# Optimization experiments

Hardware: AMD Instinct MI355X
Metric: run time of the kernel (lower is better)

The kernel has to match this reference:

```python
import jax, jax.numpy as jnp
import numpy as np

B, T, E, G, A, D, H1, H2 = 64, 500, 256, 256, 128, 400, 256, 128
MAX_STEPS, R = 500, 5


def setup_inputs() -> dict:
    key = jax.random.key(0)
    ks = jax.random.split(key, 12)
    s = lambda k, shape: jax.random.normal(k, shape, jnp.float32) * 0.05
    return dict(
        enc_feat=jax.random.normal(ks[0], (B, T, E), jnp.float32),
        W_p1=s(ks[1], (D, H1)), b_p1=jnp.zeros((H1,), jnp.float32),
        W_p2=s(ks[2], (H1, H2)), b_p2=jnp.zeros((H2,), jnp.float32),
        # GRU cell (input = prenet_out + context = H2+E)
        W_ix=s(ks[3], (H2 + E, 3 * G)), W_ih=s(ks[4], (G, 3 * G)),
        b_ix=jnp.zeros((3 * G,), jnp.float32), b_ih=jnp.zeros((3 * G,), jnp.float32),
        # Bahdanau MLP attention: v^T tanh(W_dec h + W_enc e + b)
        W_dec=s(ks[5], (G, A)), W_enc=s(ks[6], (E, A)),
        b_attn=jnp.zeros((A,), jnp.float32), v_attn=s(ks[7], (A,)),
        # output projection [G+E] -> D, softmaxed per R chunks
        W_out=s(ks[8], (G + E, D)), b_out=jnp.zeros((D,), jnp.float32),
    )


def reference(enc_feat, W_p1, b_p1, W_p2, b_p2, W_ix, W_ih, b_ix, b_ih,
              W_dec, W_enc, b_attn, v_attn, W_out, b_out):
    # precompute encoder-side attention projection once [B,T,A]
    enc_proj = enc_feat @ W_enc

    def gru_cell(x, h):
        gi = x @ W_ix + b_ix  # [B,3G]
        gh = h @ W_ih + b_ih
        i_r, i_z, i_n = jnp.split(gi, 3, axis=-1)
        h_r, h_z, h_n = jnp.split(gh, 3, axis=-1)
        r = jax.nn.sigmoid(i_r + h_r)
        z = jax.nn.sigmoid(i_z + h_z)
        n = jnp.tanh(i_n + r * h_n)
        return (1.0 - z) * n + z * h

    def step(carry, _):
        pred, h, context = carry
        # prenet (eval: no dropout)
        x = jax.nn.relu(jax.nn.relu(pred @ W_p1 + b_p1) @ W_p2 + b_p2)  # [B,H2]
        h = gru_cell(jnp.concatenate([x, context], axis=-1), h)  # [B,G]
        score = jnp.einsum('bta,a->bt',
                           jnp.tanh(enc_proj + (h @ W_dec + b_attn)[:, None, :]),
                           v_attn)  # [B,T]
        attn = jax.nn.softmax(score, axis=-1)
        context = jnp.einsum('bt,bte->be', attn, enc_feat)  # [B,E]
        raw = jnp.concatenate([h, context], axis=-1) @ W_out + b_out  # [B,D]
        pred = jax.nn.softmax(raw.reshape(B, R, D // R), axis=-1).reshape(B, D)
        return (pred, h, context), (pred, attn)

    init = (jnp.zeros((B, D), enc_feat.dtype),
            jnp.zeros((B, G), enc_feat.dtype),
            jnp.zeros((B, E), enc_feat.dtype))
    _, (pred_seq, attn_record) = jax.lax.scan(step, init, None, length=MAX_STEPS)
    # scan stacks on leading axis: [S,B,.] -> [B,S,.]
    return jnp.transpose(pred_seq, (1, 0, 2)), jnp.transpose(attn_record, (1, 0, 2))
```

## Files before the change

### kernel.cpp

```cpp
#include <hip/hip_runtime.h>
#include <math.h>

constexpr int Bb = 64, Tt = 500, Ee = 256, Gg = 256, Aa = 128, Dd = 400;
constexpr int H1 = 256, H2 = 128, STEPS = 500, Rr = 5;

__global__ __launch_bounds__(512)
void k_encproj(const float* __restrict__ enc_feat,
               const float* __restrict__ W_enc,
               float* __restrict__ enc_proj) {
  __shared__ float sFeat[16][256];
  const int b = blockIdx.x, tg = blockIdx.y;
  const int t0 = tg * 16;
  const int tid = threadIdx.x;

  #pragma unroll
  for (int i = 0; i < 8; ++i) {
    int idx = tid + i * 512;
    int r = idx >> 8, c = idx & 255;
    int t = t0 + r;
    sFeat[r][c] = (t < Tt) ? enc_feat[((size_t)b * Tt + t) * Ee + c] : 0.0f;
  }
  __syncthreads();

  const int a = tid & 127, tl = tid >> 7;
  float acc0 = 0.f, acc1 = 0.f, acc2 = 0.f, acc3 = 0.f;
  #pragma unroll 4
  for (int k = 0; k < Ee; ++k) {
    float w = W_enc[k * Aa + a];
    acc0 = fmaf(sFeat[tl][k],      w, acc0);
    acc1 = fmaf(sFeat[tl + 4][k],  w, acc1);
    acc2 = fmaf(sFeat[tl + 8][k],  w, acc2);
    acc3 = fmaf(sFeat[tl + 12][k], w, acc3);
  }
  float accs[4] = {acc0, acc1, acc2, acc3};
  #pragma unroll
  for (int i = 0; i < 4; ++i) {
    int t = t0 + tl + 4 * i;
    if (t < Tt) enc_proj[((size_t)b * Tt + t) * Aa + a] = accs[i];
  }
}


template<int QUADS, int KS>
__device__ __forceinline__ void gemv_partial(const float* __restrict__ W, const int ldW,
                                             const float* __restrict__ xl,
                                             float* __restrict__ sTmp, int tid) {
  const int q = tid & (QUADS - 1);
  const int s = tid / QUADS;
  const float* Wp = W + 4 * q + (size_t)(s * KS) * ldW;
  const float* xp = xl + s * KS;
  float4 acc = {0.f, 0.f, 0.f, 0.f};
  #pragma unroll 4
  for (int k = 0; k < KS; ++k) {
    float xv = xp[k];
    float4 w = *(const float4*)(Wp + (size_t)k * ldW);
    acc.x = fmaf(xv, w.x, acc.x);
    acc.y = fmaf(xv, w.y, acc.y);
    acc.z = fmaf(xv, w.z, acc.z);
    acc.w = fmaf(xv, w.w, acc.w);
  }
  *(float4*)&sTmp[tid * 4] = acc;
}

template<int QUADS, int NSL>
__device__ __forceinline__ float combine(const float* __restrict__ sTmp, int j) {
  float v = 0.f;
  #pragma unroll
  for (int s = 0; s < NSL; ++s)
    v += sTmp[(s * QUADS + (j >> 2)) * 4 + (j & 3)];
  return v;
}

__device__ __forceinline__ float sigmoid_acc(float x) {
  float e = __expf(-x);
  return 1.0f / (1.0f + e);
}

__device__ __forceinline__ float tanh_acc(float x) {
  float cx = fminf(9.5f, fmaxf(-9.5f, x));
  float e = __expf(2.0f * cx);
  return (e - 1.0f) / (e + 1.0f);
}

__device__ __forceinline__ float tanh_fast(float x) {
  float cx = fminf(9.5f, fmaxf(-9.5f, x));
  float e = __expf(2.0f * cx);
  return (e - 1.0f) * __builtin_amdgcn_rcpf(e + 1.0f);
}

__global__ __launch_bounds__(512, 1)
void k_decoder(const float* __restrict__ enc_feat,
               const float* __restrict__ enc_proj,
               const float* __restrict__ W_p1, const float* __restrict__ b_p1,
               const float* __restrict__ W_p2, const float* __restrict__ b_p2,
               const float* __restrict__ W_ix, const float* __restrict__ W_ih,
               const float* __restrict__ b_ix, const float* __restrict__ b_ih,
               const float* __restrict__ W_dec, const float* __restrict__ b_attn,
               const float* __restrict__ v_attn,
               const float* __restrict__ W_out, const float* __restrict__ b_out,
               float* __restrict__ pred_out, float* __restrict__ attn_out) {
  __shared__ __align__(16) float sPred[400];
  __shared__ __align__(16) float sIn[384];
  __shared__ __align__(16) float sL1[256];
  __shared__ __align__(16) float sCat[512];
  __shared__ __align__(16) float sR[256];
  __shared__ __align__(16) float sZ[256];
  __shared__ __align__(16) float sSd[128];
  __shared__ __align__(16) float sScore[512];
  __shared__ __align__(16) float sRaw[400];
  __shared__ __align__(16) float sTmpA[2048];
  __shared__ __align__(16) float sTmpB[2048];
  __shared__ float sRed[8];

  float* sH   = sCat;
  float* sCtx = sCat + 256;

  const int b = blockIdx.x;
  const int tid = threadIdx.x;
  const int lane = tid & 63, wid = tid >> 6;
  const int l4 = tid & 3;

  for (int i = tid; i < 400; i += 512) sPred[i] = 0.f;
  for (int i = tid; i < 256; i += 512) { sH[i] = 0.f; sCtx[i] = 0.f; sIn[128 + i] = 0.f; }
  __syncthreads();

  float4 vq[8];
  #pragma unroll
  for (int i = 0; i < 8; ++i) vq[i] = *(const float4*)(v_attn + 4 * (l4 + 4 * i));

  for (int t = 0; t < STEPS; ++t) {
    gemv_partial<64, 50>(W_p1, 256, sPred, sTmpA, tid);
    __syncthreads();
    if (tid < 256) {
      float v = b_p1[tid] + combine<64, 8>(sTmpA, tid);
      sL1[tid] = fmaxf(v, 0.f);
    }
    __syncthreads();

    gemv_partial<32, 16>(W_p2, 128, sL1, sTmpA, tid);
    __syncthreads();
    if (tid < 128) {
      float v = b_p2[tid] + combine<32, 16>(sTmpA, tid);
      sIn[tid] = fmaxf(v, 0.f);
    }
    __syncthreads();

    gemv_partial<64, 48>(W_ix, 768, sIn, sTmpA, tid);
    gemv_partial<64, 32>(W_ih, 768, sH, sTmpB, tid);
    __syncthreads();
    if (tid < 256) {
      float ir = b_ix[tid] + combine<64, 8>(sTmpA, tid);
      float hr = b_ih[tid] + combine<64, 8>(sTmpB, tid);
      sR[tid] = sigmoid_acc(ir + hr);
    }
    __syncthreads();

    gemv_partial<64, 48>(W_ix + 256, 768, sIn, sTmpA, tid);
    gemv_partial<64, 32>(W_ih + 256, 768, sH, sTmpB, tid);
    __syncthreads();
    if (tid < 256) {
      float iz = b_ix[256 + tid] + combine<64, 8>(sTmpA, tid);
      float hz = b_ih[256 + tid] + combine<64, 8>(sTmpB, tid);
      sZ[tid] = sigmoid_acc(iz + hz);
    }
    __syncthreads();

    gemv_partial<64, 48>(W_ix + 512, 768, sIn, sTmpA, tid);
    gemv_partial<64, 32>(W_ih + 512, 768, sH, sTmpB, tid);
    __syncthreads();
    if (tid < 256) {
      float in_ = b_ix[512 + tid] + combine<64, 8>(sTmpA, tid);
      float hn_ = b_ih[512 + tid] + combine<64, 8>(sTmpB, tid);
      float n = tanh_acc(in_ + sR[tid] * hn_);
      float z = sZ[tid];
      sH[tid] = (1.f - z) * n + z * sH[tid];
    }
    __syncthreads();

    gemv_partial<32, 16>(W_dec, 128, sH, sTmpA, tid);
    __syncthreads();
    if (tid < 128) sSd[tid] = b_attn[tid] + combine<32, 16>(sTmpA, tid);
    __syncthreads();

    {
      float4 sdq[8];
      #pragma unroll
      for (int i = 0; i < 8; ++i) sdq[i] = *(const float4*)(sSd + 4 * (l4 + 4 * i));
      const int g = tid >> 2;
      #pragma unroll
      for (int p = 0; p < 4; ++p) {
        int tt = g + (p << 7);
        float acc = 0.f;
        if (tt < Tt) {
          const float4* ep = (const float4*)(enc_proj + ((size_t)b * Tt + tt) * Aa);
          #pragma unroll
          for (int i = 0; i < 8; ++i) {
            float4 e4 = ep[l4 + 4 * i];
            acc = fmaf(vq[i].x, tanh_fast(e4.x + sdq[i].x), acc);
            acc = fmaf(vq[i].y, tanh_fast(e4.y + sdq[i].y), acc);
            acc = fmaf(vq[i].z, tanh_fast(e4.z + sdq[i].z), acc);
            acc = fmaf(vq[i].w, tanh_fast(e4.w + sdq[i].w), acc);
          }
        }
        acc += __shfl_xor(acc, 1);
        acc += __shfl_xor(acc, 2);
        if (l4 == 0 && tt < Tt) sScore[tt] = acc;
      }
      __syncthreads();
    }

    {
      float val = (tid < Tt) ? sScore[tid] : -3.0e38f;
      float m = val;
      #pragma unroll
      for (int off = 32; off >= 1; off >>= 1) m = fmaxf(m, __shfl_xor(m, off));
      if (lane == 0) sRed[wid] = m;
      __syncthreads();
      float bm = sRed[0];
      #pragma unroll
      for (int w = 1; w < 8; ++w) bm = fmaxf(bm, sRed[w]);
      float e = (tid < Tt) ? __expf(val - bm) : 0.f;
      float ssum = e;
      #pragma unroll
      for (int off = 32; off >= 1; off >>= 1) ssum += __shfl_xor(ssum, off);
      __syncthreads();
      if (lane == 0) sRed[wid] = ssum;
      __syncthreads();
      float S = 0.f;
      #pragma unroll
      for (int w = 0; w < 8; ++w) S += sRed[w];
      if (tid < Tt) {
        float attn = e / S;
        sScore[tid] = attn;
        attn_out[((size_t)b * STEPS + t) * Tt + tid] = attn;
      }
      __syncthreads();
    }

    {
      const int e4i = tid & 63, sl = tid >> 6;
      const int t0s = sl * 63;
      const int t1s = (t0s + 63 < Tt) ? (t0s + 63) : Tt;
      float4 acc = {0.f, 0.f, 0.f, 0.f};
      const float* fb = enc_feat + (size_t)b * Tt * Ee + 4 * e4i;
      #pragma unroll 4
      for (int tt = t0s; tt < t1s; ++tt) {
        float a = sScore[tt];
        float4 f = *(const float4*)(fb + (size_t)tt * Ee);
        acc.x = fmaf(a, f.x, acc.x);
        acc.y = fmaf(a, f.y, acc.y);
        acc.z = fmaf(a, f.z, acc.z);
        acc.w = fmaf(a, f.w, acc.w);
      }
      *(float4*)&sTmpA[tid * 4] = acc;
      __syncthreads();
      if (tid < 256) {
        float v = combine<64, 8>(sTmpA, tid);
        sCtx[tid] = v;
        sIn[128 + tid] = v;
      }
      __syncthreads();
    }

    {
      if (tid < 500) {
        const int s = tid / 100;
        const int q = tid - s * 100;
        const int k0 = s * 103;
        const int k1 = (s == 4) ? 512 : k0 + 103;
        const float* Wp = W_out + 4 * q;
        float4 acc = {0.f, 0.f, 0.f, 0.f};
        for (int k = k0; k < k1; ++k) {
          float xv = sCat[k];
          float4 w = *(const float4*)(Wp + (size_t)k * 400);
          acc.x = fmaf(xv, w.x, acc.x);
          acc.y = fmaf(xv, w.y, acc.y);
          acc.z = fmaf(xv, w.z, acc.z);
          acc.w = fmaf(xv, w.w, acc.w);
        }
        *(float4*)&sTmpA[tid * 4] = acc;
      }
      __syncthreads();
      if (tid < 400) {
        float v = b_out[tid];
        #pragma unroll
        for (int s2 = 0; s2 < 5; ++s2)
          v += sTmpA[(s2 * 100 + (tid >> 2)) * 4 + (tid & 3)];
        sRaw[tid] = v;
      }
      __syncthreads();
    }

    {
      if (wid < Rr) {
        int d0 = wid * 80 + lane;
        float v0 = sRaw[d0];
        float v1 = (lane < 16) ? sRaw[d0 + 64] : -3.0e38f;
        float m = fmaxf(v0, v1);
        #pragma unroll
        for (int off = 32; off >= 1; off >>= 1) m = fmaxf(m, __shfl_xor(m, off));
        float e0 = __expf(v0 - m);
        float e1 = (lane < 16) ? __expf(v1 - m) : 0.f;
        float s = e0 + e1;
        #pragma unroll
        for (int off = 32; off >= 1; off >>= 1) s += __shfl_xor(s, off);
        float inv = 1.0f / s;
        float p0 = e0 * inv;
        sPred[d0] = p0;
        pred_out[((size_t)b * STEPS + t) * Dd + d0] = p0;
        if (lane < 16) {
          float p1 = e1 * inv;
          sPred[d0 + 64] = p1;
          pred_out[((size_t)b * STEPS + t) * Dd + d0 + 64] = p1;
        }
      }
      __syncthreads();
    }
  }
}

extern "C" void kernel_launch(void* const* d_in, const int* in_sizes, int n_in,
                              void* d_out, int out_size, void* d_ws, size_t ws_size,
                              hipStream_t stream) {
  const float* enc_feat = (const float*)d_in[0];
  const float* W_p1  = (const float*)d_in[1];
  const float* b_p1  = (const float*)d_in[2];
  const float* W_p2  = (const float*)d_in[3];
  const float* b_p2  = (const float*)d_in[4];
  const float* W_ix  = (const float*)d_in[5];
  const float* W_ih  = (const float*)d_in[6];
  const float* b_ix  = (const float*)d_in[7];
  const float* b_ih  = (const float*)d_in[8];
  const float* W_dec = (const float*)d_in[9];
  const float* W_enc = (const float*)d_in[10];
  const float* b_attn= (const float*)d_in[11];
  const float* v_attn= (const float*)d_in[12];
  const float* W_out = (const float*)d_in[13];
  const float* b_out = (const float*)d_in[14];

  float* pred_out = (float*)d_out;
  float* attn_out = pred_out + (size_t)Bb * STEPS * Dd;
  float* enc_proj = (float*)d_ws;

  k_encproj<<<dim3(Bb, 32), 512, 0, stream>>>(enc_feat, W_enc, enc_proj);
  k_decoder<<<Bb, 512, 0, stream>>>(enc_feat, enc_proj,
                                    W_p1, b_p1, W_p2, b_p2,
                                    W_ix, W_ih, b_ix, b_ih,
                                    W_dec, b_attn, v_attn, W_out, b_out,
                                    pred_out, attn_out);
}
```

Baseline: 36.66 ms.

## Double decoder block to 1024 threads and fuse the three GRU gate GEMVs into one pass

The persistent per-batch decoder block grows from 512 to 1024 threads, and every GEMV stage is re-split so more threads share the K dimension. The three separate GRU gate GEMV phases, with their extra barriers, are merged into one phase where different thread ranges compute the r, z and n partials together. Biases and per-thread weight pointers are hoisted out of the step loop, and the attention score, context and output projection loops are rebalanced for the larger block. This targets the serial latency of each of the 500 recurrent steps, at the cost of higher register pressure under the 1024-thread launch bound and longer combine reductions.

```diff
diff --git a/kernel.cpp b/kernel.cpp
--- a/kernel.cpp
+++ b/kernel.cpp
@@ -1,8 +1,8 @@
 #include <hip/hip_runtime.h>
 #include <math.h>
 
-constexpr int Bb = 64, Tt = 500, Ee = 256, Gg = 256, Aa = 128, Dd = 400;
-constexpr int H1 = 256, H2 = 128, STEPS = 500, Rr = 5;
+constexpr int Bb = 64, Tt = 500, Ee = 256, Aa = 128, Dd = 400;
+constexpr int STEPS = 500, Rr = 5;
 
 __global__ __launch_bounds__(512)
 void k_encproj(const float* __restrict__ enc_feat,
@@ -40,35 +40,20 @@
   }
 }
 
-
-template<int QUADS, int KS>
-__device__ __forceinline__ void gemv_partial(const float* __restrict__ W, const int ldW,
-                                             const float* __restrict__ xl,
-                                             float* __restrict__ sTmp, int tid) {
-  const int q = tid & (QUADS - 1);
-  const int s = tid / QUADS;
-  const float* Wp = W + 4 * q + (size_t)(s * KS) * ldW;
-  const float* xp = xl + s * KS;
+template<int KS, int LDW>
+__device__ __forceinline__ float4 dotq(const float* __restrict__ Wp,
+                                       const float* __restrict__ xp) {
   float4 acc = {0.f, 0.f, 0.f, 0.f};
-  #pragma unroll 4
+  #pragma unroll
   for (int k = 0; k < KS; ++k) {
     float xv = xp[k];
-    float4 w = *(const float4*)(Wp + (size_t)k * ldW);
+    float4 w = *(const float4*)(Wp + (size_t)k * LDW);
     acc.x = fmaf(xv, w.x, acc.x);
     acc.y = fmaf(xv, w.y, acc.y);
     acc.z = fmaf(xv, w.z, acc.z);
     acc.w = fmaf(xv, w.w, acc.w);
   }
-  *(float4*)&sTmp[tid * 4] = acc;
-}
-
-template<int QUADS, int NSL>
-__device__ __forceinline__ float combine(const float* __restrict__ sTmp, int j) {
-  float v = 0.f;
-  #pragma unroll
-  for (int s = 0; s < NSL; ++s)
-    v += sTmp[(s * QUADS + (j >> 2)) * 4 + (j & 3)];
-  return v;
+  return acc;
 }
 
 __device__ __forceinline__ float sigmoid_acc(float x) {
@@ -88,7 +73,7 @@
   return (e - 1.0f) * __builtin_amdgcn_rcpf(e + 1.0f);
 }
 
-__global__ __launch_bounds__(512, 1)
+__global__ __launch_bounds__(1024)
 void k_decoder(const float* __restrict__ enc_feat,
                const float* __restrict__ enc_proj,
                const float* __restrict__ W_p1, const float* __restrict__ b_p1,
@@ -103,14 +88,11 @@
   __shared__ __align__(16) float sIn[384];
   __shared__ __align__(16) float sL1[256];
   __shared__ __align__(16) float sCat[512];
-  __shared__ __align__(16) float sR[256];
-  __shared__ __align__(16) float sZ[256];
   __shared__ __align__(16) float sSd[128];
   __shared__ __align__(16) float sScore[512];
   __shared__ __align__(16) float sRaw[400];
-  __shared__ __align__(16) float sTmpA[2048];
-  __shared__ __align__(16) float sTmpB[2048];
-  __shared__ float sRed[8];
+  __shared__ __align__(16) float sTmp[4096];
+  __shared__ float sRed[16];
 
   float* sH   = sCat;
   float* sCtx = sCat + 256;
@@ -120,66 +102,106 @@
   const int lane = tid & 63, wid = tid >> 6;
   const int l4 = tid & 3;
 
-  for (int i = tid; i < 400; i += 512) sPred[i] = 0.f;
-  for (int i = tid; i < 256; i += 512) { sH[i] = 0.f; sCtx[i] = 0.f; sIn[128 + i] = 0.f; }
-  __syncthreads();
+  for (int i = tid; i < 400; i += 1024) sPred[i] = 0.f;
+  if (tid < 256) { sH[tid] = 0.f; sCtx[tid] = 0.f; sIn[128 + tid] = 0.f; }
 
   float4 vq[8];
   #pragma unroll
   for (int i = 0; i < 8; ++i) vq[i] = *(const float4*)(v_attn + 4 * (l4 + 4 * i));
 
+  float bP1 = 0.f, bR = 0.f, bZ = 0.f, bIN = 0.f, bHN = 0.f;
+  if (tid < 256) {
+    bP1 = b_p1[tid];
+    bR  = b_ix[tid]       + b_ih[tid];
+    bZ  = b_ix[256 + tid] + b_ih[256 + tid];
+    bIN = b_ix[512 + tid];
+    bHN = b_ih[512 + tid];
+  }
+  float bP2 = 0.f, bAt = 0.f;
+  if (tid < 128) { bP2 = b_p2[tid]; bAt = b_attn[tid]; }
+  float bOut = 0.f;
+  if (tid < 400) bOut = b_out[tid];
+
+  const float* p1W = W_p1 + 4 * (tid & 63) + (size_t)((tid >> 6) * 25) * 256;
+  const float* p1x = sPred + (tid >> 6) * 25;
+  const float* p2W = W_p2 + 4 * (tid & 31) + (size_t)((tid >> 5) * 8) * 128;
+  const float* p2x = sL1 + (tid >> 5) * 8;
+  const float* p6W = W_dec + 4 * (tid & 31) + (size_t)((tid >> 5) * 8) * 128;
+  const float* p6x = sH + (tid >> 5) * 8;
+  const float* gW = W_ix;
+  const float* gx = sIn;
+  const bool gAct = tid < 960;
+  if (tid < 640) {
+    int q = tid & 127, s = tid >> 7;
+    int kbase = s * 128;
+    if (kbase < 384) { gW = W_ix + (size_t)kbase * 768 + 4 * q; gx = sIn + kbase; }
+    else             { gW = W_ih + (size_t)(kbase - 384) * 768 + 4 * q; gx = sH + (kbase - 384); }
+  } else if (tid < 832) {
+    int u = tid - 640, q = u & 63, s = u >> 6;
+    gW = W_ix + (size_t)(s * 128) * 768 + 512 + 4 * q; gx = sIn + s * 128;
+  } else if (tid < 960) {
+    int u = tid - 832, q = u & 63, s = u >> 6;
+    gW = W_ih + (size_t)(s * 128) * 768 + 512 + 4 * q; gx = sH + s * 128;
+  }
+  const int q10 = tid % 100, s10 = tid / 100;
+  const float* p10W = W_out + 4 * q10 + (size_t)(64 * s10) * 400;
+  const float* p10x = sCat + 64 * s10;
+  const int e4i = tid & 63, sl9 = tid >> 6;
+  const float* fb9 = enc_feat + (size_t)b * Tt * Ee + 4 * e4i;
+  const int t9a = sl9 * 32;
+  const int t9b = (t9a + 32 < Tt) ? t9a + 32 : Tt;
+
+  __syncthreads();
+
   for (int t = 0; t < STEPS; ++t) {
-    gemv_partial<64, 50>(W_p1, 256, sPred, sTmpA, tid);
+    { float4 a = dotq<25, 256>(p1W, p1x); *(float4*)&sTmp[tid * 4] = a; }
     __syncthreads();
     if (tid < 256) {
-      float v = b_p1[tid] + combine<64, 8>(sTmpA, tid);
+      float v = bP1;
+      #pragma unroll
+      for (int s = 0; s < 16; ++s) v += sTmp[(s * 64 + (tid >> 2)) * 4 + (tid & 3)];
       sL1[tid] = fmaxf(v, 0.f);
     }
     __syncthreads();
 
-    gemv_partial<32, 16>(W_p2, 128, sL1, sTmpA, tid);
+    { float4 a = dotq<8, 128>(p2W, p2x); *(float4*)&sTmp[tid * 4] = a; }
     __syncthreads();
     if (tid < 128) {
-      float v = b_p2[tid] + combine<32, 16>(sTmpA, tid);
+      float v = bP2;
+      #pragma unroll
+      for (int s = 0; s < 32; ++s) v += sTmp[(s * 32 + (tid >> 2)) * 4 + (tid & 3)];
       sIn[tid] = fmaxf(v, 0.f);
     }
     __syncthreads();
 
-    gemv_partial<64, 48>(W_ix, 768, sIn, sTmpA, tid);
-    gemv_partial<64, 32>(W_ih, 768, sH, sTmpB, tid);
+    if (gAct) { float4 a = dotq<128, 768>(gW, gx); *(float4*)&sTmp[tid * 4] = a; }
     __syncthreads();
     if (tid < 256) {
-      float ir = b_ix[tid] + combine<64, 8>(sTmpA, tid);
-      float hr = b_ih[tid] + combine<64, 8>(sTmpB, tid);
-      sR[tid] = sigmoid_acc(ir + hr);
-    }
-    __syncthreads();
-
-    gemv_partial<64, 48>(W_ix + 256, 768, sIn, sTmpA, tid);
-    gemv_partial<64, 32>(W_ih + 256, 768, sH, sTmpB, tid);
-    __syncthreads();
-    if (tid < 256) {
-      float iz = b_ix[256 + tid] + combine<64, 8>(sTmpA, tid);
-      float hz = b_ih[256 + tid] + combine<64, 8>(sTmpB, tid);
-      sZ[tid] = sigmoid_acc(iz + hz);
-    }
-    __syncthreads();
-
-    gemv_partial<64, 48>(W_ix + 512, 768, sIn, sTmpA, tid);
-    gemv_partial<64, 32>(W_ih + 512, 768, sH, sTmpB, tid);
-    __syncthreads();
-    if (tid < 256) {
-      float in_ = b_ix[512 + tid] + combine<64, 8>(sTmpA, tid);
-      float hn_ = b_ih[512 + tid] + combine<64, 8>(sTmpB, tid);
-      float n = tanh_acc(in_ + sR[tid] * hn_);
-      float z = sZ[tid];
+      const int qr = tid >> 2, el = tid & 3;
+      float cr = bR, cz = bZ, vin = bIN, vhn = bHN;
+      #pragma unroll
+      for (int s = 0; s < 5; ++s) cr += sTmp[(s * 128 + qr) * 4 + el];
+      #pragma unroll
+      for (int s = 0; s < 5; ++s) cz += sTmp[(s * 128 + 64 + qr) * 4 + el];
+      #pragma unroll
+      for (int s = 0; s < 3; ++s) vin += sTmp[(640 + s * 64 + qr) * 4 + el];
+      #pragma unroll
+      for (int s = 0; s < 2; ++s) vhn += sTmp[(832 + s * 64 + qr) * 4 + el];
+      float r = sigmoid_acc(cr);
+      float z = sigmoid_acc(cz);
+      float n = tanh_acc(vin + r * vhn);
       sH[tid] = (1.f - z) * n + z * sH[tid];
     }
     __syncthreads();
 
-    gemv_partial<32, 16>(W_dec, 128, sH, sTmpA, tid);
-    __syncthreads();
-    if (tid < 128) sSd[tid] = b_attn[tid] + combine<32, 16>(sTmpA, tid);
+    { float4 a = dotq<8, 128>(p6W, p6x); *(float4*)&sTmp[tid * 4] = a; }
+    __syncthreads();
+    if (tid < 128) {
+      float v = bAt;
+      #pragma unroll
+      for (int s = 0; s < 32; ++s) v += sTmp[(s * 32 + (tid >> 2)) * 4 + (tid & 3)];
+      sSd[tid] = v;
+    }
     __syncthreads();
 
     {
@@ -188,8 +210,8 @@
       for (int i = 0; i < 8; ++i) sdq[i] = *(const float4*)(sSd + 4 * (l4 + 4 * i));
       const int g = tid >> 2;
       #pragma unroll
-      for (int p = 0; p < 4; ++p) {
-        int tt = g + (p << 7);
+      for (int p = 0; p < 2; ++p) {
+        int tt = g + (p << 8);
         float acc = 0.f;
         if (tt < Tt) {
           const float4* ep = (const float4*)(enc_proj + ((size_t)b * Tt + tt) * Aa);
@@ -218,7 +240,7 @@
       __syncthreads();
       float bm = sRed[0];
       #pragma unroll
-      for (int w = 1; w < 8; ++w) bm = fmaxf(bm, sRed[w]);
+      for (int w = 1; w < 16; ++w) bm = fmaxf(bm, sRed[w]);
       float e = (tid < Tt) ? __expf(val - bm) : 0.f;
       float ssum = e;
       #pragma unroll
@@ -228,7 +250,7 @@
       __syncthreads();
       float S = 0.f;
       #pragma unroll
-      for (int w = 0; w < 8; ++w) S += sRed[w];
+      for (int w = 0; w < 16; ++w) S += sRed[w];
       if (tid < Tt) {
         float attn = e / S;
         sScore[tid] = attn;
@@ -238,58 +260,37 @@
     }
 
     {
-      const int e4i = tid & 63, sl = tid >> 6;
-      const int t0s = sl * 63;
-      const int t1s = (t0s + 63 < Tt) ? (t0s + 63) : Tt;
       float4 acc = {0.f, 0.f, 0.f, 0.f};
-      const float* fb = enc_feat + (size_t)b * Tt * Ee + 4 * e4i;
-      #pragma unroll 4
-      for (int tt = t0s; tt < t1s; ++tt) {
+      #pragma unroll 8
+      for (int tt = t9a; tt < t9b; ++tt) {
         float a = sScore[tt];
-        float4 f = *(const float4*)(fb + (size_t)tt * Ee);
+        float4 f = *(const float4*)(fb9 + (size_t)tt * Ee);
         acc.x = fmaf(a, f.x, acc.x);
         acc.y = fmaf(a, f.y, acc.y);
         acc.z = fmaf(a, f.z, acc.z);
         acc.w = fmaf(a, f.w, acc.w);
       }
-      *(float4*)&sTmpA[tid * 4] = acc;
+      *(float4*)&sTmp[tid * 4] = acc;
       __syncthreads();
       if (tid < 256) {
-        float v = combine<64, 8>(sTmpA, tid);
+        float v = 0.f;
+        #pragma unroll
+        for (int s = 0; s < 16; ++s) v += sTmp[(s * 64 + (tid >> 2)) * 4 + (tid & 3)];
         sCtx[tid] = v;
         sIn[128 + tid] = v;
       }
       __syncthreads();
     }
 
-    {
-      if (tid < 500) {
-        const int s = tid / 100;
-        const int q = tid - s * 100;
-        const int k0 = s * 103;
-        const int k1 = (s == 4) ? 512 : k0 + 103;
-        const float* Wp = W_out + 4 * q;
-        float4 acc = {0.f, 0.f, 0.f, 0.f};
-        for (int k = k0; k < k1; ++k) {
-          float xv = sCat[k];
-          float4 w = *(const float4*)(Wp + (size_t)k * 400);
-          acc.x = fmaf(xv, w.x, acc.x);
-          acc.y = fmaf(xv, w.y, acc.y);
-          acc.z = fmaf(xv, w.z, acc.z);
-          acc.w = fmaf(xv, w.w, acc.w);
-        }
-        *(float4*)&sTmpA[tid * 4] = acc;
-      }
-      __syncthreads();
-      if (tid < 400) {
-        float v = b_out[tid];
-        #pragma unroll
-        for (int s2 = 0; s2 < 5; ++s2)
-          v += sTmpA[(s2 * 100 + (tid >> 2)) * 4 + (tid & 3)];
-        sRaw[tid] = v;
-      }
-      __syncthreads();
-    }
+    if (tid < 800) { float4 a = dotq<64, 400>(p10W, p10x); *(float4*)&sTmp[tid * 4] = a; }
+    __syncthreads();
+    if (tid < 400) {
+      float v = bOut;
+      #pragma unroll
+      for (int s = 0; s < 8; ++s) v += sTmp[(s * 100 + (tid >> 2)) * 4 + (tid & 3)];
+      sRaw[tid] = v;
+    }
+    __syncthreads();
 
     {
       if (wid < Rr) {
@@ -343,9 +344,9 @@
   float* enc_proj = (float*)d_ws;
 
   k_encproj<<<dim3(Bb, 32), 512, 0, stream>>>(enc_feat, W_enc, enc_proj);
-  k_decoder<<<Bb, 512, 0, stream>>>(enc_feat, enc_proj,
-                                    W_p1, b_p1, W_p2, b_p2,
-                                    W_ix, W_ih, b_ix, b_ih,
-                                    W_dec, b_attn, v_attn, W_out, b_out,
-                                    pred_out, attn_out);
-}
+  k_decoder<<<Bb, 1024, 0, stream>>>(enc_feat, enc_proj,
+                                     W_p1, b_p1, W_p2, b_p2,
+                                     W_ix, W_ih, b_ix, b_ih,
+                                     W_dec, b_attn, v_attn, W_out, b_out,
+                                     pred_out, attn_out);
+}
```

After: 89.56 ms. 2.44x slower.

## Split decoder across 128 cooperative blocks with group barriers and transposed weights

Applied to the files above, without the earlier changes.

Replaces the one-block-per-batch-row decoder with a cooperative launch of 128 blocks. Each group of 16 blocks handles 8 batch rows jointly, so every block computes a 16-column slice of each GEMV for all 8 rows. The blocks in a group exchange intermediates through global staging buffers and sync via atomic flag barriers. Attention is split in halves over T between block pairs and merged with a max/sum softmax combine. Weights are pre-transposed for contiguous k-major float4 reads. The aim is to spread the serial per-step weight traffic over more CUs and reuse each weight load across 8 rows, at the cost of many global barriers per step.

```diff
diff --git a/kernel.cpp b/kernel.cpp
--- a/kernel.cpp
+++ b/kernel.cpp
@@ -1,8 +1,40 @@
 #include <hip/hip_runtime.h>
 #include <math.h>
 
-constexpr int Bb = 64, Tt = 500, Ee = 256, Gg = 256, Aa = 128, Dd = 400;
-constexpr int H1 = 256, H2 = 128, STEPS = 500, Rr = 5;
+constexpr int Bb = 64, Tt = 500, Ee = 256, Aa = 128, Dd = 400;
+constexpr int STEPS = 500;
+
+constexpr size_t WS_ENCPROJ = 0;
+constexpr size_t WS_WT      = 4096000;
+constexpr size_t WS_STAGE   = WS_WT + 864256;
+constexpr size_t WS_CNT     = WS_STAGE + 8 * 16384;
+constexpr int OT_P1  = 0;
+constexpr int OT_P2  = 102400;
+constexpr int OT_DEC = 135168;
+constexpr int OT_G   = 167936;
+constexpr int OT_OUT = 659456;
+constexpr int SL1 = 0, SH = 2048, SCTXP = 4096, SRAW = 8192, SPRED = 11392, SSTAT = 14592;
+
+__global__ __launch_bounds__(512)
+void k_transpose(const float* __restrict__ W_p1, const float* __restrict__ W_p2,
+                 const float* __restrict__ W_dec, const float* __restrict__ W_ix,
+                 const float* __restrict__ W_ih, const float* __restrict__ W_out,
+                 float* __restrict__ WT) {
+  int i = blockIdx.x * 512 + threadIdx.x;
+  if (i < 102400) { int j = i / 400, k = i % 400; WT[OT_P1 + i] = W_p1[k * 256 + j]; return; }
+  i -= 102400;
+  if (i < 32768) { int j = i / 256, k = i % 256; WT[OT_P2 + i] = W_p2[k * 128 + j]; return; }
+  i -= 32768;
+  if (i < 32768) { int j = i / 256, k = i % 256; WT[OT_DEC + i] = W_dec[k * 128 + j]; return; }
+  i -= 32768;
+  if (i < 491520) {
+    int gc = i / 640, k = i % 640;
+    WT[OT_G + i] = (k < 384) ? W_ix[(size_t)k * 768 + gc] : W_ih[(size_t)(k - 384) * 768 + gc];
+    return;
+  }
+  i -= 491520;
+  if (i < 204800) { int j = i / 512, k = i % 512; WT[OT_OUT + i] = W_out[k * 400 + j]; }
+}
 
 __global__ __launch_bounds__(512)
 void k_encproj(const float* __restrict__ enc_feat,
@@ -12,7 +44,6 @@
   const int b = blockIdx.x, tg = blockIdx.y;
   const int t0 = tg * 16;
   const int tid = threadIdx.x;
-
   #pragma unroll
   for (int i = 0; i < 8; ++i) {
     int idx = tid + i * 512;
@@ -21,7 +52,6 @@
     sFeat[r][c] = (t < Tt) ? enc_feat[((size_t)b * Tt + t) * Ee + c] : 0.0f;
   }
   __syncthreads();
-
   const int a = tid & 127, tl = tid >> 7;
   float acc0 = 0.f, acc1 = 0.f, acc2 = 0.f, acc3 = 0.f;
   #pragma unroll 4
@@ -40,177 +70,314 @@
   }
 }
 
-
-template<int QUADS, int KS>
-__device__ __forceinline__ void gemv_partial(const float* __restrict__ W, const int ldW,
-                                             const float* __restrict__ xl,
-                                             float* __restrict__ sTmp, int tid) {
-  const int q = tid & (QUADS - 1);
-  const int s = tid / QUADS;
-  const float* Wp = W + 4 * q + (size_t)(s * KS) * ldW;
-  const float* xp = xl + s * KS;
-  float4 acc = {0.f, 0.f, 0.f, 0.f};
-  #pragma unroll 4
-  for (int k = 0; k < KS; ++k) {
-    float xv = xp[k];
-    float4 w = *(const float4*)(Wp + (size_t)k * ldW);
-    acc.x = fmaf(xv, w.x, acc.x);
-    acc.y = fmaf(xv, w.y, acc.y);
-    acc.z = fmaf(xv, w.z, acc.z);
-    acc.w = fmaf(xv, w.w, acc.w);
-  }
-  *(float4*)&sTmp[tid * 4] = acc;
-}
-
-template<int QUADS, int NSL>
-__device__ __forceinline__ float combine(const float* __restrict__ sTmp, int j) {
-  float v = 0.f;
-  #pragma unroll
-  for (int s = 0; s < NSL; ++s)
-    v += sTmp[(s * QUADS + (j >> 2)) * 4 + (j & 3)];
-  return v;
-}
-
 __device__ __forceinline__ float sigmoid_acc(float x) {
   float e = __expf(-x);
   return 1.0f / (1.0f + e);
 }
-
 __device__ __forceinline__ float tanh_acc(float x) {
   float cx = fminf(9.5f, fmaxf(-9.5f, x));
   float e = __expf(2.0f * cx);
   return (e - 1.0f) / (e + 1.0f);
 }
-
 __device__ __forceinline__ float tanh_fast(float x) {
   float cx = fminf(9.5f, fmaxf(-9.5f, x));
   float e = __expf(2.0f * cx);
   return (e - 1.0f) * __builtin_amdgcn_rcpf(e + 1.0f);
 }
 
-__global__ __launch_bounds__(512, 1)
+__device__ __forceinline__ void gsync(unsigned* __restrict__ slots, int i16, int tid, unsigned ep) {
+  __syncthreads();
+  if (tid == 0)
+    __hip_atomic_store(&slots[i16 * 16], ep, __ATOMIC_RELEASE, __HIP_MEMORY_SCOPE_AGENT);
+  if (tid < 16)
+    while (__hip_atomic_load(&slots[tid * 16], __ATOMIC_RELAXED, __HIP_MEMORY_SCOPE_AGENT) < ep) { }
+  __threadfence();
+  __syncthreads();
+}
+
+__device__ __forceinline__ void psync(unsigned* __restrict__ self, unsigned* __restrict__ peer,
+                                      int tid, unsigned ep) {
+  __syncthreads();
+  if (tid == 0) {
+    __hip_atomic_store(self, ep, __ATOMIC_RELEASE, __HIP_MEMORY_SCOPE_AGENT);
+    while (__hip_atomic_load(peer, __ATOMIC_RELAXED, __HIP_MEMORY_SCOPE_AGENT) < ep) { }
+  }
+  __threadfence();
+  __syncthreads();
+}
+
+__global__ __launch_bounds__(512)
 void k_decoder(const float* __restrict__ enc_feat,
                const float* __restrict__ enc_proj,
-               const float* __restrict__ W_p1, const float* __restrict__ b_p1,
-               const float* __restrict__ W_p2, const float* __restrict__ b_p2,
-               const float* __restrict__ W_ix, const float* __restrict__ W_ih,
+               const float* __restrict__ WT,
+               float* __restrict__ stage, unsigned* __restrict__ cnt,
+               const float* __restrict__ b_p1, const float* __restrict__ b_p2,
                const float* __restrict__ b_ix, const float* __restrict__ b_ih,
-               const float* __restrict__ W_dec, const float* __restrict__ b_attn,
-               const float* __restrict__ v_attn,
-               const float* __restrict__ W_out, const float* __restrict__ b_out,
+               const float* __restrict__ b_attn, const float* __restrict__ v_attn,
+               const float* __restrict__ b_out,
                float* __restrict__ pred_out, float* __restrict__ attn_out) {
-  __shared__ __align__(16) float sPred[400];
-  __shared__ __align__(16) float sIn[384];
-  __shared__ __align__(16) float sL1[256];
-  __shared__ __align__(16) float sCat[512];
-  __shared__ __align__(16) float sR[256];
-  __shared__ __align__(16) float sZ[256];
-  __shared__ __align__(16) float sSd[128];
-  __shared__ __align__(16) float sScore[512];
-  __shared__ __align__(16) float sRaw[400];
-  __shared__ __align__(16) float sTmpA[2048];
-  __shared__ __align__(16) float sTmpB[2048];
+  __shared__ __align__(16) float predL[3200];
+  __shared__ __align__(16) float inL[5120];
+  __shared__ __align__(16) float l1L[2048];
+  __shared__ __align__(16) float sdL[128];
+  __shared__ __align__(16) float rawL[3200];
+  __shared__ __align__(16) float scoreL[256];
+  __shared__ __align__(16) float sTmp[2048];
   __shared__ float sRed[8];
 
-  float* sH   = sCat;
-  float* sCtx = sCat + 256;
-
-  const int b = blockIdx.x;
+  const int bid = blockIdx.x;
+  const int g = bid & 7, i16 = bid >> 3;
+  const int ri = i16 >> 1, hf = i16 & 1;
+  const int rowg = 8 * g + ri;
   const int tid = threadIdx.x;
   const int lane = tid & 63, wid = tid >> 6;
   const int l4 = tid & 3;
 
-  for (int i = tid; i < 400; i += 512) sPred[i] = 0.f;
-  for (int i = tid; i < 256; i += 512) { sH[i] = 0.f; sCtx[i] = 0.f; sIn[128 + i] = 0.f; }
-  __syncthreads();
+  float* stg = stage + (size_t)g * 16384;
+  unsigned* cslot = cnt + g * 1024;
+  unsigned* pfSelf = cnt + g * 1024 + 512 + (ri * 2 + hf) * 16;
+  unsigned* pfPeer = cnt + g * 1024 + 512 + (ri * 2 + (hf ^ 1)) * 16;
+
+  const float* WT_p1  = WT + OT_P1;
+  const float* WT_p2  = WT + OT_P2;
+  const float* WT_dec = WT + OT_DEC;
+  const float* WT_g   = WT + OT_G;
+  const float* WT_out = WT + OT_OUT;
+
+  for (int i = tid; i < 3200; i += 512) predL[i] = 0.f;
+  for (int i = tid; i < 5120; i += 512) inL[i] = 0.f;
 
   float4 vq[8];
   #pragma unroll
   for (int i = 0; i < 8; ++i) vq[i] = *(const float4*)(v_attn + 4 * (l4 + 4 * i));
 
+  const int c1 = tid & 15, r1 = (tid >> 4) & 7, s1 = tid >> 7;
+  const float* w1 = WT_p1 + (size_t)(16 * i16 + c1) * 400 + 100 * s1;
+  const int xo1 = r1 * 400 + 100 * s1;
+  float bP1 = 0.f;
+  if (tid < 128) bP1 = b_p1[16 * i16 + (tid & 15)];
+
+  const int cp2 = tid >> 3, r2 = tid & 7;
+  const float* w2a = WT_p2 + (size_t)(2 * cp2) * 256;
+  const float* w2b = w2a + 256;
+  const int xo2 = r2 * 256;
+  const int dst2 = r2 * 640 + 2 * cp2;
+  const float bP2a = b_p2[2 * cp2], bP2b = b_p2[2 * cp2 + 1];
+
+  const bool gAct = tid < 384;
+  int gc0 = 0, gc1 = 0, sg = 0, rg = 0, sti0 = 0, sti1 = 0, xog = 0;
+  if (gAct) {
+    int c2 = tid % 24; rg = (tid / 24) & 7; sg = tid / 192;
+    int lc0 = 2 * c2, lc1 = lc0 + 1;
+    gc0 = (lc0 >> 4) * 256 + 16 * i16 + (lc0 & 15);
+    gc1 = (lc1 >> 4) * 256 + 16 * i16 + (lc1 & 15);
+    sti0 = sg * 384 + lc0 * 8 + rg;
+    sti1 = sg * 384 + lc1 * 8 + rg;
+    xog = rg * 640 + (sg ? 384 : 0);
+  }
+  const float* wg0 = WT_g + (size_t)gc0 * 640 + (sg ? 384 : 0);
+  const float* wg1 = WT_g + (size_t)gc1 * 640 + (sg ? 384 : 0);
+  float bR = 0.f, bZ = 0.f, bIN = 0.f, bHN = 0.f;
+  int colC = 0, rC = 0, holdOff = 0, stH = 0;
+  if (tid < 128) {
+    int hc = tid >> 3; rC = tid & 7; colC = 16 * i16 + hc;
+    bR  = b_ix[colC]       + b_ih[colC];
+    bZ  = b_ix[256 + colC] + b_ih[256 + colC];
+    bIN = b_ix[512 + colC];
+    bHN = b_ih[512 + colC];
+    holdOff = rC * 640 + 384 + colC;
+    stH = colC * 8 + rC;
+  }
+
+  const int c6 = tid & 127, s6 = tid >> 7;
+  const float* w6 = WT_dec + (size_t)c6 * 256 + 64 * s6;
+  const int xo6 = ri * 640 + 384 + 64 * s6;
+  float bAt = 0.f;
+  if (tid < 128) bAt = b_attn[tid];
+
+  const float* encp = enc_proj + ((size_t)rowg * Tt + 250 * hf) * Aa;
+  const int e9q = tid & 63, sl9 = tid >> 6;
+  const int t9a = sl9 * 32;
+  const int t9b = (t9a + 32 < 250) ? t9a + 32 : 250;
+  const float* encf = enc_feat + ((size_t)rowg * Tt + 250 * hf) * Ee + 4 * e9q;
+
+  const bool a10 = tid < 400;
+  int c25 = 0, r10 = 0, s10 = 0;
+  if (a10) { c25 = tid % 25; r10 = (tid / 25) & 7; s10 = tid / 200; }
+  const float* w10 = WT_out + (size_t)(25 * i16 + c25) * 512 + 256 * s10;
+  const int xo10 = r10 * 640 + (s10 ? 128 : 384);
+  float bO = 0.f;
+  int stRAW = 0;
+  if (tid < 200) {
+    int cw = tid % 25, rw = tid / 25;
+    bO = b_out[25 * i16 + cw];
+    stRAW = (25 * i16 + cw) * 8 + rw;
+  }
+
+  const int nch = hf ? 2 : 3, ch0 = hf ? 3 : 0;
+
+  __syncthreads();
+
+  unsigned ep = 0;
+
   for (int t = 0; t < STEPS; ++t) {
-    gemv_partial<64, 50>(W_p1, 256, sPred, sTmpA, tid);
-    __syncthreads();
-    if (tid < 256) {
-      float v = b_p1[tid] + combine<64, 8>(sTmpA, tid);
-      sL1[tid] = fmaxf(v, 0.f);
-    }
-    __syncthreads();
-
-    gemv_partial<32, 16>(W_p2, 128, sL1, sTmpA, tid);
+    if (t > 0) {
+      {
+        int i4 = tid;
+        float4 v = *(const float4*)(stg + SPRED + 4 * i4);
+        int col = (4 * i4) >> 3, rb = (4 * i4) & 7;
+        predL[(rb + 0) * 400 + col] = v.x; predL[(rb + 1) * 400 + col] = v.y;
+        predL[(rb + 2) * 400 + col] = v.z; predL[(rb + 3) * 400 + col] = v.w;
+      }
+      if (tid < 288) {
+        int i4 = tid + 512;
+        float4 v = *(const float4*)(stg + SPRED + 4 * i4);
+        int col = (4 * i4) >> 3, rb = (4 * i4) & 7;
+        predL[(rb + 0) * 400 + col] = v.x; predL[(rb + 1) * 400 + col] = v.y;
+        predL[(rb + 2) * 400 + col] = v.z; predL[(rb + 3) * 400 + col] = v.w;
+      }
+      __syncthreads();
+    }
+
+    {
+      float acc = 0.f;
+      #pragma unroll 5
+      for (int k = 0; k < 100; k += 4) {
+        float4 w4 = *(const float4*)(w1 + k);
+        float4 x4 = *(const float4*)(predL + xo1 + k);
+        acc = fmaf(w4.x, x4.x, acc); acc = fmaf(w4.y, x4.y, acc);
+        acc = fmaf(w4.z, x4.z, acc); acc = fmaf(w4.w, x4.w, acc);
+      }
+      sTmp[tid] = acc;
+    }
     __syncthreads();
     if (tid < 128) {
-      float v = b_p2[tid] + combine<32, 16>(sTmpA, tid);
-      sIn[tid] = fmaxf(v, 0.f);
-    }
-    __syncthreads();
-
-    gemv_partial<64, 48>(W_ix, 768, sIn, sTmpA, tid);
-    gemv_partial<64, 32>(W_ih, 768, sH, sTmpB, tid);
-    __syncthreads();
-    if (tid < 256) {
-      float ir = b_ix[tid] + combine<64, 8>(sTmpA, tid);
-      float hr = b_ih[tid] + combine<64, 8>(sTmpB, tid);
-      sR[tid] = sigmoid_acc(ir + hr);
-    }
-    __syncthreads();
-
-    gemv_partial<64, 48>(W_ix + 256, 768, sIn, sTmpA, tid);
-    gemv_partial<64, 32>(W_ih + 256, 768, sH, sTmpB, tid);
-    __syncthreads();
-    if (tid < 256) {
-      float iz = b_ix[256 + tid] + combine<64, 8>(sTmpA, tid);
-      float hz = b_ih[256 + tid] + combine<64, 8>(sTmpB, tid);
-      sZ[tid] = sigmoid_acc(iz + hz);
-    }
-    __syncthreads();
-
-    gemv_partial<64, 48>(W_ix + 512, 768, sIn, sTmpA, tid);
-    gemv_partial<64, 32>(W_ih + 512, 768, sH, sTmpB, tid);
-    __syncthreads();
-    if (tid < 256) {
-      float in_ = b_ix[512 + tid] + combine<64, 8>(sTmpA, tid);
-      float hn_ = b_ih[512 + tid] + combine<64, 8>(sTmpB, tid);
-      float n = tanh_acc(in_ + sR[tid] * hn_);
-      float z = sZ[tid];
-      sH[tid] = (1.f - z) * n + z * sH[tid];
-    }
-    __syncthreads();
-
-    gemv_partial<32, 16>(W_dec, 128, sH, sTmpA, tid);
-    __syncthreads();
-    if (tid < 128) sSd[tid] = b_attn[tid] + combine<32, 16>(sTmpA, tid);
+      float v = bP1 + sTmp[tid] + sTmp[tid + 128] + sTmp[tid + 256] + sTmp[tid + 384];
+      stg[SL1 + (16 * i16 + (tid & 15)) * 8 + (tid >> 4)] = fmaxf(v, 0.f);
+    }
+    gsync(cslot, i16, tid, ++ep);
+
+    {
+      int i4 = tid;
+      float4 v = *(const float4*)(stg + SL1 + 4 * i4);
+      int col = (4 * i4) >> 3, rb = (4 * i4) & 7;
+      l1L[(rb + 0) * 256 + col] = v.x; l1L[(rb + 1) * 256 + col] = v.y;
+      l1L[(rb + 2) * 256 + col] = v.z; l1L[(rb + 3) * 256 + col] = v.w;
+    }
+    __syncthreads();
+
+    {
+      float a0 = 0.f, a1 = 0.f;
+      #pragma unroll 8
+      for (int k = 0; k < 256; k += 4) {
+        float4 x4 = *(const float4*)(l1L + xo2 + k);
+        float4 wA = *(const float4*)(w2a + k);
+        float4 wB = *(const float4*)(w2b + k);
+        a0 = fmaf(wA.x, x4.x, a0); a0 = fmaf(wA.y, x4.y, a0);
+        a0 = fmaf(wA.z, x4.z, a0); a0 = fmaf(wA.w, x4.w, a0);
+        a1 = fmaf(wB.x, x4.x, a1); a1 = fmaf(wB.y, x4.y, a1);
+        a1 = fmaf(wB.z, x4.z, a1); a1 = fmaf(wB.w, x4.w, a1);
+      }
+      inL[dst2]     = fmaxf(a0 + bP2a, 0.f);
+      inL[dst2 + 1] = fmaxf(a1 + bP2b, 0.f);
+    }
+    __syncthreads();
+
+    if (gAct) {
+      float a0 = 0.f, a1 = 0.f;
+      if (sg == 0) {
+        #pragma unroll 8
+        for (int k = 0; k < 384; k += 4) {
+          float4 x4 = *(const float4*)(inL + xog + k);
+          float4 wA = *(const float4*)(wg0 + k);
+          float4 wB = *(const float4*)(wg1 + k);
+          a0 = fmaf(wA.x, x4.x, a0); a0 = fmaf(wA.y, x4.y, a0);
+          a0 = fmaf(wA.z, x4.z, a0); a0 = fmaf(wA.w, x4.w, a0);
+          a1 = fmaf(wB.x, x4.x, a1); a1 = fmaf(wB.y, x4.y, a1);
+          a1 = fmaf(wB.z, x4.z, a1); a1 = fmaf(wB.w, x4.w, a1);
+        }
+      } else {
+        #pragma unroll 8
+        for (int k = 0; k < 256; k += 4) {
+          float4 x4 = *(const float4*)(inL + xog + k);
+          float4 wA = *(const float4*)(wg0 + k);
+          float4 wB = *(const float4*)(wg1 + k);
+          a0 = fmaf(wA.x, x4.x, a0); a0 = fmaf(wA.y, x4.y, a0);
+          a0 = fmaf(wA.z, x4.z, a0); a0 = fmaf(wA.w, x4.w, a0);
+          a1 = fmaf(wB.x, x4.x, a1); a1 = fmaf(wB.y, x4.y, a1);
+          a1 = fmaf(wB.z, x4.z, a1); a1 = fmaf(wB.w, x4.w, a1);
+        }
+      }
+      sTmp[sti0] = a0;
+      sTmp[sti1] = a1;
+    }
+    __syncthreads();
+    if (tid < 128) {
+      int hc = tid >> 3;
+      float rpre = bR  + sTmp[hc * 8 + rC]        + sTmp[384 + hc * 8 + rC];
+      float zpre = bZ  + sTmp[(16 + hc) * 8 + rC] + sTmp[384 + (16 + hc) * 8 + rC];
+      float inp  = bIN + sTmp[(32 + hc) * 8 + rC];
+      float hnp  = bHN + sTmp[384 + (32 + hc) * 8 + rC];
+      float rgt = sigmoid_acc(rpre);
+      float zgt = sigmoid_acc(zpre);
+      float n   = tanh_acc(inp + rgt * hnp);
+      stg[SH + stH] = (1.f - zgt) * n + zgt * inL[holdOff];
+    }
+    gsync(cslot, i16, tid, ++ep);
+
+    {
+      int i4 = tid;
+      float4 v = *(const float4*)(stg + SH + 4 * i4);
+      int col = (4 * i4) >> 3, rb = (4 * i4) & 7;
+      inL[(rb + 0) * 640 + 384 + col] = v.x; inL[(rb + 1) * 640 + 384 + col] = v.y;
+      inL[(rb + 2) * 640 + 384 + col] = v.z; inL[(rb + 3) * 640 + 384 + col] = v.w;
+    }
+    __syncthreads();
+
+    {
+      float acc = 0.f;
+      #pragma unroll 8
+      for (int k = 0; k < 64; k += 4) {
+        float4 w4 = *(const float4*)(w6 + k);
+        float4 x4 = *(const float4*)(inL + xo6 + k);
+        acc = fmaf(w4.x, x4.x, acc); acc = fmaf(w4.y, x4.y, acc);
+        acc = fmaf(w4.z, x4.z, acc); acc = fmaf(w4.w, x4.w, acc);
+      }
+      sTmp[s6 * 128 + c6] = acc;
+    }
+    __syncthreads();
+    if (tid < 128)
+      sdL[tid] = bAt + sTmp[tid] + sTmp[128 + tid] + sTmp[256 + tid] + sTmp[384 + tid];
     __syncthreads();
 
     {
       float4 sdq[8];
       #pragma unroll
-      for (int i = 0; i < 8; ++i) sdq[i] = *(const float4*)(sSd + 4 * (l4 + 4 * i));
-      const int g = tid >> 2;
-      #pragma unroll
-      for (int p = 0; p < 4; ++p) {
-        int tt = g + (p << 7);
-        float acc = 0.f;
-        if (tt < Tt) {
-          const float4* ep = (const float4*)(enc_proj + ((size_t)b * Tt + tt) * Aa);
+      for (int i = 0; i < 8; ++i) sdq[i] = *(const float4*)(sdL + 4 * (l4 + 4 * i));
+      if (tid < 500) {
+        #pragma unroll
+        for (int p = 0; p < 2; ++p) {
+          int ttl = p * 125 + (tid >> 2);
+          const float* epn = encp + (size_t)ttl * 128 + 4 * l4;
+          float acc = 0.f;
           #pragma unroll
           for (int i = 0; i < 8; ++i) {
-            float4 e4 = ep[l4 + 4 * i];
+            float4 e4 = *(const float4*)(epn + 16 * i);
             acc = fmaf(vq[i].x, tanh_fast(e4.x + sdq[i].x), acc);
             acc = fmaf(vq[i].y, tanh_fast(e4.y + sdq[i].y), acc);
             acc = fmaf(vq[i].z, tanh_fast(e4.z + sdq[i].z), acc);
             acc = fmaf(vq[i].w, tanh_fast(e4.w + sdq[i].w), acc);
           }
+          acc += __shfl_xor(acc, 1);
+          acc += __shfl_xor(acc, 2);
+          if (l4 == 0) scoreL[ttl] = acc;
         }
-        acc += __shfl_xor(acc, 1);
-        acc += __shfl_xor(acc, 2);
-        if (l4 == 0 && tt < Tt) sScore[tt] = acc;
-      }
-      __syncthreads();
-    }
-
-    {
-      float val = (tid < Tt) ? sScore[tid] : -3.0e38f;
+      }
+    }
+    __syncthreads();
+
+    {
+      float val = (tid < 250) ? scoreL[tid] : -3.0e38f;
       float m = val;
       #pragma unroll
       for (int off = 32; off >= 1; off >>= 1) m = fmaxf(m, __shfl_xor(m, off));
@@ -219,103 +386,123 @@
       float bm = sRed[0];
       #pragma unroll
       for (int w = 1; w < 8; ++w) bm = fmaxf(bm, sRed[w]);
-      float e = (tid < Tt) ? __expf(val - bm) : 0.f;
-      float ssum = e;
-      #pragma unroll
-      for (int off = 32; off >= 1; off >>= 1) ssum += __shfl_xor(ssum, off);
+      float e = (tid < 250) ? __expf(val - bm) : 0.f;
+      float lS = e;
+      #pragma unroll
+      for (int off = 32; off >= 1; off >>= 1) lS += __shfl_xor(lS, off);
       __syncthreads();
-      if (lane == 0) sRed[wid] = ssum;
+      if (lane == 0) sRed[wid] = lS;
       __syncthreads();
-      float S = 0.f;
-      #pragma unroll
-      for (int w = 0; w < 8; ++w) S += sRed[w];
-      if (tid < Tt) {
-        float attn = e / S;
-        sScore[tid] = attn;
-        attn_out[((size_t)b * STEPS + t) * Tt + tid] = attn;
-      }
-      __syncthreads();
-    }
-
-    {
-      const int e4i = tid & 63, sl = tid >> 6;
-      const int t0s = sl * 63;
-      const int t1s = (t0s + 63 < Tt) ? (t0s + 63) : Tt;
+      if (tid == 0) {
+        float S = 0.f;
+        #pragma unroll
+        for (int w = 0; w < 8; ++w) S += sRed[w];
+        stg[SSTAT + (ri * 2 + hf) * 2]     = bm;
+        stg[SSTAT + (ri * 2 + hf) * 2 + 1] = S;
+      }
+      psync(pfSelf, pfPeer, tid, (unsigned)(t + 1));
+      float m2 = stg[SSTAT + (ri * 2 + (hf ^ 1)) * 2];
+      float S2 = stg[SSTAT + (ri * 2 + (hf ^ 1)) * 2 + 1];
+      float S1v = stg[SSTAT + (ri * 2 + hf) * 2 + 1];
+      float M = fmaxf(bm, m2);
+      float Sg = S1v * __expf(bm - M) + S2 * __expf(m2 - M);
+      if (tid < 250) {
+        float attn = __expf(val - M) / Sg;
+        scoreL[tid] = attn;
+        attn_out[((size_t)rowg * STEPS + t) * Tt + 250 * hf + tid] = attn;
+      }
+    }
+    __syncthreads();
+
+    {
       float4 acc = {0.f, 0.f, 0.f, 0.f};
-      const float* fb = enc_feat + (size_t)b * Tt * Ee + 4 * e4i;
-      #pragma unroll 4
-      for (int tt = t0s; tt < t1s; ++tt) {
-        float a = sScore[tt];
-        float4 f = *(const float4*)(fb + (size_t)tt * Ee);
-        acc.x = fmaf(a, f.x, acc.x);
-        acc.y = fmaf(a, f.y, acc.y);
-        acc.z = fmaf(a, f.z, acc.z);
-        acc.w = fmaf(a, f.w, acc.w);
-      }
-      *(float4*)&sTmpA[tid * 4] = acc;
-      __syncthreads();
-      if (tid < 256) {
-        float v = combine<64, 8>(sTmpA, tid);
-        sCtx[tid] = v;
-        sIn[128 + tid] = v;
-      }
-      __syncthreads();
-    }
-
-    {
-      if (tid < 500) {
-        const int s = tid / 100;
-        const int q = tid - s * 100;
-        const int k0 = s * 103;
-        const int k1 = (s == 4) ? 512 : k0 + 103;
-        const float* Wp = W_out + 4 * q;
-        float4 acc = {0.f, 0.f, 0.f, 0.f};
-        for (int k = k0; k < k1; ++k) {
-          float xv = sCat[k];
-          float4 w = *(const float4*)(Wp + (size_t)k * 400);
-          acc.x = fmaf(xv, w.x, acc.x);
-          acc.y = fmaf(xv, w.y, acc.y);
-          acc.z = fmaf(xv, w.z, acc.z);
-          acc.w = fmaf(xv, w.w, acc.w);
-        }
-        *(float4*)&sTmpA[tid * 4] = acc;
-      }
-      __syncthreads();
-      if (tid < 400) {
-        float v = b_out[tid];
-        #pragma unroll
-        for (int s2 = 0; s2 < 5; ++s2)
-          v += sTmpA[(s2 * 100 + (tid >> 2)) * 4 + (tid & 3)];
-        sRaw[tid] = v;
-      }
-      __syncthreads();
-    }
-
-    {
-      if (wid < Rr) {
-        int d0 = wid * 80 + lane;
-        float v0 = sRaw[d0];
-        float v1 = (lane < 16) ? sRaw[d0 + 64] : -3.0e38f;
-        float m = fmaxf(v0, v1);
-        #pragma unroll
-        for (int off = 32; off >= 1; off >>= 1) m = fmaxf(m, __shfl_xor(m, off));
-        float e0 = __expf(v0 - m);
-        float e1 = (lane < 16) ? __expf(v1 - m) : 0.f;
-        float s = e0 + e1;
-        #pragma unroll
-        for (int off = 32; off >= 1; off >>= 1) s += __shfl_xor(s, off);
-        float inv = 1.0f / s;
-        float p0 = e0 * inv;
-        sPred[d0] = p0;
-        pred_out[((size_t)b * STEPS + t) * Dd + d0] = p0;
-        if (lane < 16) {
-          float p1 = e1 * inv;
-          sPred[d0 + 64] = p1;
-          pred_out[((size_t)b * STEPS + t) * Dd + d0 + 64] = p1;
-        }
-      }
-      __syncthreads();
-    }
+      const float* fb = encf + (size_t)t9a * 256;
+      for (int tt = t9a; tt < t9b; ++tt) {
+        float a = scoreL[tt];
+        float4 f = *(const float4*)fb;
+        fb += 256;
+        acc.x = fmaf(a, f.x, acc.x); acc.y = fmaf(a, f.y, acc.y);
+        acc.z = fmaf(a, f.z, acc.z); acc.w = fmaf(a, f.w, acc.w);
+      }
+      *(float4*)&sTmp[tid * 4] = acc;
+    }
+    __syncthreads();
+    if (tid < 64) {
+      float4 v = {0.f, 0.f, 0.f, 0.f};
+      #pragma unroll
+      for (int s = 0; s < 8; ++s) {
+        float4 u = *(const float4*)&sTmp[(s * 64 + tid) * 4];
+        v.x += u.x; v.y += u.y; v.z += u.z; v.w += u.w;
+      }
+      *(float4*)&stg[SCTXP + hf * 2048 + ri * 256 + 4 * tid] = v;
+    }
+    gsync(cslot, i16, tid, ++ep);
+
+    {
+      int rr = tid >> 6, e4 = (tid & 63) * 4;
+      float4 a = *(const float4*)(stg + SCTXP + rr * 256 + e4);
+      float4 b = *(const float4*)(stg + SCTXP + 2048 + rr * 256 + e4);
+      float4 v = {a.x + b.x, a.y + b.y, a.z + b.z, a.w + b.w};
+      *(float4*)(inL + rr * 640 + 128 + e4) = v;
+    }
+    __syncthreads();
+
+    if (a10) {
+      float acc = 0.f;
+      #pragma unroll 8
+      for (int k = 0; k < 256; k += 4) {
+        float4 w4 = *(const float4*)(w10 + k);
+        float4 x4 = *(const float4*)(inL + xo10 + k);
+        acc = fmaf(w4.x, x4.x, acc); acc = fmaf(w4.y, x4.y, acc);
+        acc = fmaf(w4.z, x4.z, acc); acc = fmaf(w4.w, x4.w, acc);
+      }
+      sTmp[tid] = acc;
+    }
+    __syncthreads();
+    if (tid < 200)
+      stg[SRAW + stRAW] = bO + sTmp[tid] + sTmp[tid + 200];
+    gsync(cslot, i16, tid, ++ep);
+
+    {
+      int i4 = tid;
+      float4 v = *(const float4*)(stg + SRAW + 4 * i4);
+      int col = (4 * i4) >> 3, rb = (4 * i4) & 7;
+      rawL[(rb + 0) * 400 + col] = v.x; rawL[(rb + 1) * 400 + col] = v.y;
+      rawL[(rb + 2) * 400 + col] = v.z; rawL[(rb + 3) * 400 + col] = v.w;
+    }
+    if (tid < 288) {
+      int i4 = tid + 512;
+      float4 v = *(const float4*)(stg + SRAW + 4 * i4);
+      int col = (4 * i4) >> 3, rb = (4 * i4) & 7;
+      rawL[(rb + 0) * 400 + col] = v.x; rawL[(rb + 1) * 400 + col] = v.y;
+      rawL[(rb + 2) * 400 + col] = v.z; rawL[(rb + 3) * 400 + col] = v.w;
+    }
+    __syncthreads();
+
+    if (wid < nch) {
+      int ch = ch0 + wid;
+      int d0 = ch * 80 + lane;
+      float v0 = rawL[ri * 400 + d0];
+      float v1 = (lane < 16) ? rawL[ri * 400 + d0 + 64] : -3.0e38f;
+      float m = fmaxf(v0, v1);
+      #pragma unroll
+      for (int off = 32; off >= 1; off >>= 1) m = fmaxf(m, __shfl_xor(m, off));
+      float e0 = __expf(v0 - m);
+      float e1 = (lane < 16) ? __expf(v1 - m) : 0.f;
+      float s = e0 + e1;
+      #pragma unroll
+      for (int off = 32; off >= 1; off >>= 1) s += __shfl_xor(s, off);
+      float inv = 1.0f / s;
+      float p0 = e0 * inv;
+      stg[SPRED + d0 * 8 + ri] = p0;
+      pred_out[((size_t)rowg * STEPS + t) * Dd + d0] = p0;
+      if (lane < 16) {
+        float p1 = e1 * inv;
+        stg[SPRED + (d0 + 64) * 8 + ri] = p1;
+        pred_out[((size_t)rowg * STEPS + t) * Dd + d0 + 64] = p1;
+      }
+    }
+    gsync(cslot, i16, tid, ++ep);
   }
 }
 
@@ -340,12 +527,23 @@
 
   float* pred_out = (float*)d_out;
   float* attn_out = pred_out + (size_t)Bb * STEPS * Dd;
-  float* enc_proj = (float*)d_ws;
-
+
+  float* ws = (float*)d_ws;
+  float* enc_proj = ws + WS_ENCPROJ;
+  float* WT       = ws + WS_WT;
+  float* stage    = ws + WS_STAGE;
+  unsigned* cnt   = (unsigned*)(ws + WS_CNT);
+
+  (void)hipMemsetAsync(cnt, 0, 8192 * sizeof(unsigned), stream);
+  k_transpose<<<1688, 512, 0, stream>>>(W_p1, W_p2, W_dec, W_ix, W_ih, W_out, WT);
   k_encproj<<<dim3(Bb, 32), 512, 0, stream>>>(enc_feat, W_enc, enc_proj);
-  k_decoder<<<Bb, 512, 0, stream>>>(enc_feat, enc_proj,
-                                    W_p1, b_p1, W_p2, b_p2,
-                                    W_ix, W_ih, b_ix, b_ih,
-                                    W_dec, b_attn, v_attn, W_out, b_out,
-                                    pred_out, attn_out);
-}
+
+  void* args[] = {
+    (void*)&enc_feat, (void*)&enc_proj, (void*)&WT, (void*)&stage, (void*)&cnt,
+    (void*)&b_p1, (void*)&b_p2, (void*)&b_ix, (void*)&b_ih,
+    (void*)&b_attn, (void*)&v_attn, (void*)&b_out,
+    (void*)&pred_out, (void*)&attn_out
+  };
+  (void)hipLaunchCooperativeKernel(reinterpret_cast<const void*>(k_decoder),
+                                   dim3(128), dim3(512), args, 0, stream);
+}
```

New measurement: 89.00 ms. 143% more time.
